# Performance work log

Hardware: AMD Instinct MI355X
Metric: run time of the kernel (lower is better)

## Reference

```python
import jax, jax.numpy as jnp
import numpy as np

K_CLASSES = 5   # num support classes (5-way)
N_SHOT = 5      # supports per class


def setup_inputs() -> dict:
    key = jax.random.key(0)
    k0, k1, k2, k3 = jax.random.split(key, 4)
    b, bs, c, h, w = 32, K_CLASSES * N_SHOT, 512, 14, 14
    dk, dv = 128, 128
    return {
        "support_features": jax.random.normal(k0, (bs, c, h, w), jnp.float32),
        "query_features": jax.random.normal(k1, (b, c, h, w), jnp.float32),
        "support_labels": jnp.repeat(jnp.arange(K_CLASSES), N_SHOT).astype(jnp.int32),
        "W_qk": jax.random.normal(k2, (dk, c), jnp.float32) * 0.02,  # 1x1 conv weight
        "W_v": jax.random.normal(k3, (dv, c), jnp.float32) * 0.02,   # 1x1 conv weight
    }


def reference(support_features, query_features, support_labels, W_qk, W_v):
    scale = 1.0  # 1/temperature, temperature=1.0
    # 1x1 convs == channel-mixing einsums
    query_q = jnp.einsum('bchw,dc->bdhw', query_features, W_qk)
    query_v = jnp.einsum('bchw,dc->bdhw', query_features, W_v)
    supp_k = jnp.einsum('nchw,dc->ndhw', support_features, W_qk)
    supp_v = jnpveinsum = jnp.einsum('nchw,dc->ndhw', support_features, W_v)
    supp_v = jnpveinsum
    b, cv, h, w = query_v.shape

    # similarity over all supports: [b,h,w,n,i,j] (contracts dim_key)
    sim = jnp.einsum('bchw,ncij->bhwnij', query_q, supp_k) * scale

    # per-class masked softmax over the (n,i,j) axes restricted to that class's
    # supports == index_select + softmax in the original loop (labels balanced).
    cls_mask = support_labels[None, :] == jnp.arange(K_CLASSES)[:, None]  # [K,n]
    neg = jnp.finfo(sim.dtype).min
    sim_k = jnp.where(cls_mask[:, None, None, None, :, None, None], sim[None], neg)  # [K,b,h,w,n,i,j]
    attn = jax.nn.softmax(sim_k.reshape(K_CLASSES, b, h, w, -1), axis=-1)
    attn = attn.reshape(sim_k.shape)  # masked-out entries -> exactly 0

    # weighted sum of support values: [K,b,c,h,w]
    out = jnp.einsum('kbhwnij,ncij->kbchw', attn, supp_v)
    prototypes = jnp.transpose(out, (1, 0, 2, 3, 4)).reshape(b, K_CLASSES, -1)  # b k (c h w)
    query_v_flat = query_v.reshape(b, 1, -1)  # b () (c h w)
    return prototypes, query_v_flat
```

## Files before the change

### kernel.cpp

```cpp
#include <hip/hip_runtime.h>
#include <cstdint>
#include <cstddef>

#define NB   32
#define NSUP 25
#define KCLS 5
#define NC   512
#define ND   128
#define NP   196
#define JS   208
#define SHIFT 8.0f

#define KPITCH 272
#define KTILE  (16 * KPITCH)
#define KBUF   (2 * KTILE)
#define VPITCH 80
#define VBUF   (128 * VPITCH)
#define BUFSZ  (KBUF + VBUF)

typedef __attribute__((ext_vector_type(8))) short short8;
typedef __attribute__((ext_vector_type(4))) float floatx4;

__device__ inline short f2bf(float x) {
  union { float f; uint32_t u; } v; v.f = x;
  uint32_t r = (v.u + 0x7FFFu + ((v.u >> 16) & 1u)) >> 16;
  return (short)(r & 0xFFFFu);
}
__device__ inline uint32_t pk2(float a, float b) {
  return (uint32_t)(uint16_t)f2bf(a) | ((uint32_t)(uint16_t)f2bf(b) << 16);
}

__global__ __launch_bounds__(256) void wconv_kernel(
    const float* __restrict__ Wqk, const float* __restrict__ Wv,
    uint16_t* __restrict__ Whi)
{
  const int f = (blockIdx.x * 256 + (int)threadIdx.x) * 8;
  const float* src = (f < ND * NC) ? (Wqk + f) : (Wv + f - ND * NC);
  short8 hv;
  #pragma unroll
  for (int i = 0; i < 8; ++i) hv[i] = f2bf(src[i]);
  *(short8*)(Whi + f) = hv;
}

__global__ __launch_bounds__(256) void gemm_kernel(
    const float* __restrict__ supp, const float* __restrict__ qry,
    const uint16_t* __restrict__ Whi,
    uint16_t* __restrict__ Qt, uint16_t* __restrict__ Kt,
    uint16_t* __restrict__ Vt, float* __restrict__ outVq)
{
  __shared__ uint16_t xs[16 * 520];
  const int bx = blockIdx.x;
  const int t16 = bx % 13, img = bx / 13;
  const int tid = (int)threadIdx.x;
  const int w = tid >> 6, lane = tid & 63, ln = lane & 15, q = lane >> 4;
  const int d0 = w * 32;
  const int p0 = t16 * 16;

  const float* __restrict__ X = (img < NB)
      ? (qry  + (size_t)img * NC * NP)
      : (supp + (size_t)(img - NB) * NC * NP);

  #pragma unroll
  for (int k = 0; k < 4; ++k) {
    const int id = k * 256 + tid;
    const int cp = id >> 2;
    const int pq = id & 3;
    int pg = p0 + pq * 4; if (pg > NP - 4) pg = NP - 4;
    const floatx4 fa = *(const floatx4*)(X + (2 * cp) * NP + pg);
    const floatx4 fb = *(const floatx4*)(X + (2 * cp + 1) * NP + pg);
    #pragma unroll
    for (int i = 0; i < 4; ++i)
      *((uint32_t*)xs + (pq * 4 + i) * 260 + cp) = pk2(fa[i], fb[i]);
  }
  __syncthreads();

  floatx4 aQ[2], aV[2];
  #pragma unroll
  for (int nt = 0; nt < 2; ++nt) {
    aQ[nt] = (floatx4){0.f, 0.f, 0.f, 0.f};
    aV[nt] = (floatx4){0.f, 0.f, 0.f, 0.f};
  }

  for (int ks = 0; ks < 16; ++ks) {
    const short8 xh = *(const short8*)&xs[ln * 520 + ks * 32 + q * 8];
    #pragma unroll
    for (int nt = 0; nt < 2; ++nt) {
      const size_t wr = (size_t)(d0 + nt * 16 + ln) * NC + ks * 32 + q * 8;
      const short8 wqh = *(const short8*)(Whi + wr);
      aQ[nt] = __builtin_amdgcn_mfma_f32_16x16x32_bf16(xh, wqh, aQ[nt], 0, 0, 0);
      const short8 wvh = *(const short8*)(Whi + (size_t)ND * NC + wr);
      aV[nt] = __builtin_amdgcn_mfma_f32_16x16x32_bf16(wvh, xh, aV[nt], 0, 0, 0);
    }
  }

  if (img < NB) {
    #pragma unroll
    for (int nt = 0; nt < 2; ++nt)
      #pragma unroll
      for (int rr = 0; rr < 4; ++rr) {
        const int p = p0 + q * 4 + rr;
        if (p < NP)
          Qt[((size_t)img * NP + p) * ND + d0 + nt * 16 + ln] = (uint16_t)f2bf(aQ[nt][rr]);
      }
  } else {
    const int n = img - NB;
    #pragma unroll
    for (int nt = 0; nt < 2; ++nt)
      #pragma unroll
      for (int rr = 0; rr < 4; ++rr) {
        const int p = p0 + q * 4 + rr;
        Kt[((size_t)n * JS + p) * ND + d0 + nt * 16 + ln] = (uint16_t)f2bf(aQ[nt][rr]);
      }
  }
  const int p = p0 + ln;
  if (img < NB) {
    if (p < NP) {
      #pragma unroll
      for (int nt = 0; nt < 2; ++nt)
        #pragma unroll
        for (int rr = 0; rr < 4; ++rr)
          outVq[((size_t)img * ND + d0 + nt * 16 + q * 4 + rr) * NP + p] = aV[nt][rr];
    }
  } else {
    const int n = img - NB;
    #pragma unroll
    for (int nt = 0; nt < 2; ++nt)
      #pragma unroll
      for (int rr = 0; rr < 4; ++rr)
        Vt[((size_t)n * ND + d0 + nt * 16 + q * 4 + rr) * JS + p] = (uint16_t)f2bf(aV[nt][rr]);
  }
}

__global__ __launch_bounds__(256, 2) void attn_kernel(
    const uint16_t* __restrict__ Qt, const uint16_t* __restrict__ Kt,
    const uint16_t* __restrict__ Vt, const int* __restrict__ labels,
    float* __restrict__ out)
{
  __shared__ __align__(16) char smem[2 * BUFSZ];

  const int bx = blockIdx.x;
  const int pt = bx % 13;
  const int rem = bx / 13;
  const int kc = rem % KCLS;
  const int b0 = (rem / KCLS) * 4;
  const int p0 = pt * 16;
  const int tid = (int)threadIdx.x;
  const int w = tid >> 6, lane = tid & 63, ln = lane & 15, q = lane >> 4;
  const int b = b0 + w;

  const int myl = (lane < NSUP) ? labels[lane] : -1;
  unsigned long long m = __ballot(myl == kc);
  int clsPack = 0;
  #pragma unroll
  for (int s = 0; s < 5; ++s) {
    const int n = (m != 0ull) ? (int)__builtin_ctzll(m) : 0;
    clsPack |= n << (6 * s);
    m &= (m - 1);
  }

  short8 aq[4];
  {
    int p = p0 + ln; if (p > NP - 1) p = NP - 1;
    const uint16_t* base = Qt + ((size_t)b * NP + p) * ND + q * 8;
    #pragma unroll
    for (int ks = 0; ks < 4; ++ks) aq[ks] = *(const short8*)(base + ks * 32);
  }

  floatx4 acc[8];
  #pragma unroll
  for (int dt = 0; dt < 8; ++dt) acc[dt] = (floatx4){0.f, 0.f, 0.f, 0.f};
  float Ssum = 0.f;

  const int alo = (ln + ((q & 1) << 5)) << 2;
  const bool hiTile = (q >= 2);

  int4 pf[4];
  {
    int nk[2], j0k[2], nv[2], jv[2];
    #pragma unroll
    for (int t = 0; t < 2; ++t) {
      const int tile16 = t;
      int s = tile16 / 13;
      j0k[t] = (tile16 - s * 13) * 16;
      if (s > 4) s = 4;
      nk[t] = (clsPack >> (6 * s)) & 63;
    }
    #pragma unroll
    for (int h = 0; h < 2; ++h) {
      const int ch = h * 16;
      int sv = ch / JS, jvv = ch - sv * JS;
      if (sv > 4) { sv = 4; jvv = 192; }
      nv[h] = (clsPack >> (6 * sv)) & 63;
      jv[h] = jvv;
    }
    #pragma unroll
    for (int pass = 0; pass < 4; ++pass) {
      const int slot = pass * 256 + tid;
      if (pass < 2) {
        const int t = slot >> 8, r = (slot >> 4) & 15, sc = slot & 15;
        pf[pass] = *(const int4*)(Kt + ((size_t)(nk[t] * JS + j0k[t] + r)) * ND + sc * 8);
      } else {
        const int vs = slot - 512;
        const int h = vs >> 8, d = (vs >> 1) & 127, sc2 = vs & 1;
        pf[pass] = *(const int4*)(Vt + ((size_t)(nv[h] * ND + d)) * JS + jv[h] + sc2 * 8);
      }
    }
    char* db = smem;
    #pragma unroll
    for (int pass = 0; pass < 4; ++pass) {
      const int slot = pass * 256 + tid;
      if (pass < 2) {
        const int t = slot >> 8, r = (slot >> 4) & 15, sc = slot & 15;
        *(int4*)(db + t * KTILE + r * KPITCH + sc * 16) = pf[pass];
      } else {
        const int vs = slot - 512;
        const int h = vs >> 8, d = (vs >> 1) & 127, sc2 = vs & 1;
        *(int4*)(db + KBUF + d * VPITCH + (h * 2 + sc2) * 16) = pf[pass];
      }
    }
  }
  __syncthreads();

  for (int it = 0; it < 33; ++it) {
    const int nb = it + 1;
    int nk[2], j0k[2], nv[2], jv[2];
    if (nb < 33) {
      #pragma unroll
      for (int t = 0; t < 2; ++t) {
        const int tile16 = nb * 2 + t;
        int s = tile16 / 13;
        j0k[t] = (tile16 - s * 13) * 16;
        if (s > 4) s = 4;
        nk[t] = (clsPack >> (6 * s)) & 63;
      }
      #pragma unroll
      for (int h = 0; h < 2; ++h) {
        const int ch = nb * 32 + h * 16;
        int sv = ch / JS, jvv = ch - sv * JS;
        if (sv > 4) { sv = 4; jvv = 192; }
        nv[h] = (clsPack >> (6 * sv)) & 63;
        jv[h] = jvv;
      }
      #pragma unroll
      for (int pass = 0; pass < 4; ++pass) {
        const int slot = pass * 256 + tid;
        if (pass < 2) {
          const int t = slot >> 8, r = (slot >> 4) & 15, sc = slot & 15;
          pf[pass] = *(const int4*)(Kt + ((size_t)(nk[t] * JS + j0k[t] + r)) * ND + sc * 8);
        } else {
          const int vs = slot - 512;
          const int h = vs >> 8, d = (vs >> 1) & 127, sc2 = vs & 1;
          pf[pass] = *(const int4*)(Vt + ((size_t)(nv[h] * ND + d)) * JS + jv[h] + sc2 * 8);
        }
      }
    }

    const char* kb = smem + (it & 1) * BUFSZ;
    const char* vb = kb + KBUF;

    short8 av[8];
    #pragma unroll
    for (int dt = 0; dt < 8; ++dt)
      av[dt] = *(const short8*)(vb + (dt * 16 + ln) * VPITCH + q * 16);

    short8 bk[2][4];
    #pragma unroll
    for (int t = 0; t < 2; ++t)
      #pragma unroll
      for (int ks = 0; ks < 4; ++ks)
        bk[t][ks] = *(const short8*)(kb + t * KTILE + ln * KPITCH + ks * 64 + q * 16);

    floatx4 e0, e1;
    #pragma unroll
    for (int t = 0; t < 2; ++t) {
      const int tile16 = it * 2 + t;
      const int s = tile16 / 13;
      const int j0 = (tile16 - s * 13) * 16;
      const bool tval = (s < 5);
      floatx4 d4 = {0.f, 0.f, 0.f, 0.f};
      #pragma unroll
      for (int ks = 0; ks < 4; ++ks)
        d4 = __builtin_amdgcn_mfma_f32_16x16x32_bf16(bk[t][ks], aq[ks], d4, 0, 0, 0);
      floatx4 ev;
      #pragma unroll
      for (int r = 0; r < 4; ++r) {
        const int j = j0 + q * 4 + r;
        const float e = (tval && j < NP) ? __expf(d4[r] - SHIFT) : 0.f;
        ev[r] = e;
        Ssum += e;
      }
      if (t == 0) e0 = ev; else e1 = ev;
    }

    short8 bp;
    #pragma unroll
    for (int r = 0; r < 4; ++r) {
      const uint32_t pe = pk2(e0[r], e1[r]);
      const int lo = __builtin_amdgcn_ds_bpermute(alo, (int)pe);
      const int hi = __builtin_amdgcn_ds_bpermute(alo + 64, (int)pe);
      bp[r]     = (short)(uint16_t)(hiTile ? (lo >> 16) : (lo & 0xFFFF));
      bp[4 + r] = (short)(uint16_t)(hiTile ? (hi >> 16) : (hi & 0xFFFF));
    }

    #pragma unroll
    for (int dt = 0; dt < 8; ++dt)
      acc[dt] = __builtin_amdgcn_mfma_f32_16x16x32_bf16(av[dt], bp, acc[dt], 0, 0, 0);

    if (nb < 33) {
      char* db = smem + (nb & 1) * BUFSZ;
      #pragma unroll
      for (int pass = 0; pass < 4; ++pass) {
        const int slot = pass * 256 + tid;
        if (pass < 2) {
          const int t = slot >> 8, r = (slot >> 4) & 15, sc = slot & 15;
          *(int4*)(db + t * KTILE + r * KPITCH + sc * 16) = pf[pass];
        } else {
          const int vs = slot - 512;
          const int h = vs >> 8, d = (vs >> 1) & 127, sc2 = vs & 1;
          *(int4*)(db + KBUF + d * VPITCH + (h * 2 + sc2) * 16) = pf[pass];
        }
      }
    }
    __syncthreads();
  }

  float sv = Ssum;
  sv += __shfl_xor(sv, 16);
  sv += __shfl_xor(sv, 32);
  const float inv = 1.f / sv;
  const int pp = p0 + ln;
  if (pp < NP) {
    float* ob = out + ((size_t)(b * KCLS + kc) * ND + q * 4) * NP + pp;
    #pragma unroll
    for (int dt = 0; dt < 8; ++dt)
      #pragma unroll
      for (int rr = 0; rr < 4; ++rr)
        ob[(size_t)(dt * 16 + rr) * NP] = acc[dt][rr] * inv;
  }
}

extern "C" void kernel_launch(void* const* d_in, const int* in_sizes, int n_in,
                              void* d_out, int out_size, void* d_ws, size_t ws_size,
                              hipStream_t stream) {
  const float* supp   = (const float*)d_in[0];
  const float* qry    = (const float*)d_in[1];
  const int*   labels = (const int*)d_in[2];
  const float* Wqk    = (const float*)d_in[3];
  const float* Wv     = (const float*)d_in[4];
  float* out = (float*)d_out;

  uint16_t* Whi = (uint16_t*)d_ws;
  uint16_t* Qt  = Whi + (size_t)2 * ND * NC;
  uint16_t* Kt  = Qt  + (size_t)NB * NP * ND;
  uint16_t* Vt  = Kt  + (size_t)NSUP * JS * ND;
  float* outVq = out + (size_t)NB * KCLS * ND * NP;

  wconv_kernel<<<64, 256, 0, stream>>>(Wqk, Wv, Whi);
  gemm_kernel<<<741, 256, 0, stream>>>(supp, qry, Whi, Qt, Kt, Vt, outVq);
  attn_kernel<<<520, 256, 0, stream>>>(Qt, Kt, Vt, labels, out);
}
```

Before: 161.4 us.

## Load K/V MFMA fragments directly from global into registers, dropping LDS staging

Replaces the double-buffered shared-memory staging of K and V tiles with per-wave direct global loads of MFMA fragments into registers. Two register sets are ping-ponged so the next chunk is fetched while the current one is computed. This removes LDS writes/reads and all per-iteration __syncthreads, at the cost of each of the four waves redundantly fetching the same K/V data from global/L2 and of higher register pressure.

```diff
diff --git a/kernel.cpp b/kernel.cpp
--- a/kernel.cpp
+++ b/kernel.cpp
@@ -10,13 +10,6 @@
 #define NP   196
 #define JS   208
 #define SHIFT 8.0f
-
-#define KPITCH 272
-#define KTILE  (16 * KPITCH)
-#define KBUF   (2 * KTILE)
-#define VPITCH 80
-#define VBUF   (128 * VPITCH)
-#define BUFSZ  (KBUF + VBUF)
 
 typedef __attribute__((ext_vector_type(8))) short short8;
 typedef __attribute__((ext_vector_type(4))) float floatx4;
@@ -131,13 +124,74 @@
   }
 }
 
+
+#define LOAD_FRAGS(BK, AV, CH) do {                                            \
+    _Pragma("unroll")                                                          \
+    for (int t_ = 0; t_ < 2; ++t_) {                                           \
+      const int tile16_ = (CH) * 2 + t_;                                       \
+      int s_ = tile16_ / 13;                                                   \
+      const int j0_ = (tile16_ - s_ * 13) * 16;                                \
+      if (s_ > 4) s_ = 4;                                                      \
+      const int n_ = (clsPack >> (6 * s_)) & 63;                               \
+      const uint16_t* kr_ = Kt + ((size_t)(n_ * JS + j0_ + ln)) * ND + q * 8;  \
+      _Pragma("unroll")                                                        \
+      for (int ks_ = 0; ks_ < 4; ++ks_)                                        \
+        BK[t_][ks_] = *(const short8*)(kr_ + ks_ * 32);                        \
+    }                                                                          \
+    {                                                                          \
+      const int h_ = q >> 1;                                                   \
+      const int ch_ = (CH) * 32 + h_ * 16;                                     \
+      int sv_ = ch_ / JS, jv_ = ch_ - sv_ * JS;                                \
+      if (sv_ > 4) { sv_ = 4; jv_ = 192; }                                     \
+      const int n_ = (clsPack >> (6 * sv_)) & 63;                              \
+      const uint16_t* vr_ = Vt + ((size_t)n_ * ND + ln) * JS + jv_ + (q & 1) * 8; \
+      _Pragma("unroll")                                                        \
+      for (int dt_ = 0; dt_ < 8; ++dt_)                                        \
+        AV[dt_] = *(const short8*)(vr_ + (size_t)(dt_ * 16) * JS);             \
+    }                                                                          \
+  } while (0)
+
+#define COMPUTE_CHUNK(BK, AV, CH) do {                                         \
+    floatx4 e0_, e1_;                                                          \
+    _Pragma("unroll")                                                          \
+    for (int t_ = 0; t_ < 2; ++t_) {                                           \
+      const int tile16_ = (CH) * 2 + t_;                                       \
+      const int s_ = tile16_ / 13;                                             \
+      const int j0_ = (tile16_ - s_ * 13) * 16;                                \
+      const bool tval_ = (s_ < 5);                                             \
+      floatx4 d4_ = {0.f, 0.f, 0.f, 0.f};                                      \
+      _Pragma("unroll")                                                        \
+      for (int ks_ = 0; ks_ < 4; ++ks_)                                        \
+        d4_ = __builtin_amdgcn_mfma_f32_16x16x32_bf16(BK[t_][ks_], aq[ks_], d4_, 0, 0, 0); \
+      floatx4 ev_;                                                             \
+      _Pragma("unroll")                                                        \
+      for (int r_ = 0; r_ < 4; ++r_) {                                         \
+        const int j_ = j0_ + q * 4 + r_;                                       \
+        const float e_ = (tval_ && j_ < NP) ? __expf(d4_[r_] - SHIFT) : 0.f;   \
+        ev_[r_] = e_;                                                          \
+        Ssum += e_;                                                            \
+      }                                                                        \
+      if (t_ == 0) e0_ = ev_; else e1_ = ev_;                                  \
+    }                                                                          \
+    short8 bp_;                                                                \
+    _Pragma("unroll")                                                          \
+    for (int r_ = 0; r_ < 4; ++r_) {                                           \
+      const uint32_t pe_ = pk2(e0_[r_], e1_[r_]);                              \
+      const int lo_ = __builtin_amdgcn_ds_bpermute(alo, (int)pe_);             \
+      const int hi_ = __builtin_amdgcn_ds_bpermute(alo + 64, (int)pe_);        \
+      bp_[r_]     = (short)(uint16_t)(hiTile ? (lo_ >> 16) : (lo_ & 0xFFFF));  \
+      bp_[4 + r_] = (short)(uint16_t)(hiTile ? (hi_ >> 16) : (hi_ & 0xFFFF));  \
+    }                                                                          \
+    _Pragma("unroll")                                                          \
+    for (int dt_ = 0; dt_ < 8; ++dt_)                                          \
+      acc[dt_] = __builtin_amdgcn_mfma_f32_16x16x32_bf16(AV[dt_], bp_, acc[dt_], 0, 0, 0); \
+  } while (0)
+
 __global__ __launch_bounds__(256, 2) void attn_kernel(
     const uint16_t* __restrict__ Qt, const uint16_t* __restrict__ Kt,
     const uint16_t* __restrict__ Vt, const int* __restrict__ labels,
     float* __restrict__ out)
 {
-  __shared__ __align__(16) char smem[2 * BUFSZ];
-
   const int bx = blockIdx.x;
   const int pt = bx % 13;
   const int rem = bx / 13;
@@ -174,155 +228,15 @@
   const int alo = (ln + ((q & 1) << 5)) << 2;
   const bool hiTile = (q >= 2);
 
-  int4 pf[4];
-  {
-    int nk[2], j0k[2], nv[2], jv[2];
-    #pragma unroll
-    for (int t = 0; t < 2; ++t) {
-      const int tile16 = t;
-      int s = tile16 / 13;
-      j0k[t] = (tile16 - s * 13) * 16;
-      if (s > 4) s = 4;
-      nk[t] = (clsPack >> (6 * s)) & 63;
-    }
-    #pragma unroll
-    for (int h = 0; h < 2; ++h) {
-      const int ch = h * 16;
-      int sv = ch / JS, jvv = ch - sv * JS;
-      if (sv > 4) { sv = 4; jvv = 192; }
-      nv[h] = (clsPack >> (6 * sv)) & 63;
-      jv[h] = jvv;
-    }
-    #pragma unroll
-    for (int pass = 0; pass < 4; ++pass) {
-      const int slot = pass * 256 + tid;
-      if (pass < 2) {
-        const int t = slot >> 8, r = (slot >> 4) & 15, sc = slot & 15;
-        pf[pass] = *(const int4*)(Kt + ((size_t)(nk[t] * JS + j0k[t] + r)) * ND + sc * 8);
-      } else {
-        const int vs = slot - 512;
-        const int h = vs >> 8, d = (vs >> 1) & 127, sc2 = vs & 1;
-        pf[pass] = *(const int4*)(Vt + ((size_t)(nv[h] * ND + d)) * JS + jv[h] + sc2 * 8);
-      }
-    }
-    char* db = smem;
-    #pragma unroll
-    for (int pass = 0; pass < 4; ++pass) {
-      const int slot = pass * 256 + tid;
-      if (pass < 2) {
-        const int t = slot >> 8, r = (slot >> 4) & 15, sc = slot & 15;
-        *(int4*)(db + t * KTILE + r * KPITCH + sc * 16) = pf[pass];
-      } else {
-        const int vs = slot - 512;
-        const int h = vs >> 8, d = (vs >> 1) & 127, sc2 = vs & 1;
-        *(int4*)(db + KBUF + d * VPITCH + (h * 2 + sc2) * 16) = pf[pass];
-      }
-    }
-  }
-  __syncthreads();
-
-  for (int it = 0; it < 33; ++it) {
-    const int nb = it + 1;
-    int nk[2], j0k[2], nv[2], jv[2];
-    if (nb < 33) {
-      #pragma unroll
-      for (int t = 0; t < 2; ++t) {
-        const int tile16 = nb * 2 + t;
-        int s = tile16 / 13;
-        j0k[t] = (tile16 - s * 13) * 16;
-        if (s > 4) s = 4;
-        nk[t] = (clsPack >> (6 * s)) & 63;
-      }
-      #pragma unroll
-      for (int h = 0; h < 2; ++h) {
-        const int ch = nb * 32 + h * 16;
-        int sv = ch / JS, jvv = ch - sv * JS;
-        if (sv > 4) { sv = 4; jvv = 192; }
-        nv[h] = (clsPack >> (6 * sv)) & 63;
-        jv[h] = jvv;
-      }
-      #pragma unroll
-      for (int pass = 0; pass < 4; ++pass) {
-        const int slot = pass * 256 + tid;
-        if (pass < 2) {
-          const int t = slot >> 8, r = (slot >> 4) & 15, sc = slot & 15;
-          pf[pass] = *(const int4*)(Kt + ((size_t)(nk[t] * JS + j0k[t] + r)) * ND + sc * 8);
-        } else {
-          const int vs = slot - 512;
-          const int h = vs >> 8, d = (vs >> 1) & 127, sc2 = vs & 1;
-          pf[pass] = *(const int4*)(Vt + ((size_t)(nv[h] * ND + d)) * JS + jv[h] + sc2 * 8);
-        }
-      }
-    }
-
-    const char* kb = smem + (it & 1) * BUFSZ;
-    const char* vb = kb + KBUF;
-
-    short8 av[8];
-    #pragma unroll
-    for (int dt = 0; dt < 8; ++dt)
-      av[dt] = *(const short8*)(vb + (dt * 16 + ln) * VPITCH + q * 16);
-
-    short8 bk[2][4];
-    #pragma unroll
-    for (int t = 0; t < 2; ++t)
-      #pragma unroll
-      for (int ks = 0; ks < 4; ++ks)
-        bk[t][ks] = *(const short8*)(kb + t * KTILE + ln * KPITCH + ks * 64 + q * 16);
-
-    floatx4 e0, e1;
-    #pragma unroll
-    for (int t = 0; t < 2; ++t) {
-      const int tile16 = it * 2 + t;
-      const int s = tile16 / 13;
-      const int j0 = (tile16 - s * 13) * 16;
-      const bool tval = (s < 5);
-      floatx4 d4 = {0.f, 0.f, 0.f, 0.f};
-      #pragma unroll
-      for (int ks = 0; ks < 4; ++ks)
-        d4 = __builtin_amdgcn_mfma_f32_16x16x32_bf16(bk[t][ks], aq[ks], d4, 0, 0, 0);
-      floatx4 ev;
-      #pragma unroll
-      for (int r = 0; r < 4; ++r) {
-        const int j = j0 + q * 4 + r;
-        const float e = (tval && j < NP) ? __expf(d4[r] - SHIFT) : 0.f;
-        ev[r] = e;
-        Ssum += e;
-      }
-      if (t == 0) e0 = ev; else e1 = ev;
-    }
-
-    short8 bp;
-    #pragma unroll
-    for (int r = 0; r < 4; ++r) {
-      const uint32_t pe = pk2(e0[r], e1[r]);
-      const int lo = __builtin_amdgcn_ds_bpermute(alo, (int)pe);
-      const int hi = __builtin_amdgcn_ds_bpermute(alo + 64, (int)pe);
-      bp[r]     = (short)(uint16_t)(hiTile ? (lo >> 16) : (lo & 0xFFFF));
-      bp[4 + r] = (short)(uint16_t)(hiTile ? (hi >> 16) : (hi & 0xFFFF));
-    }
-
-    #pragma unroll
-    for (int dt = 0; dt < 8; ++dt)
-      acc[dt] = __builtin_amdgcn_mfma_f32_16x16x32_bf16(av[dt], bp, acc[dt], 0, 0, 0);
-
-    if (nb < 33) {
-      char* db = smem + (nb & 1) * BUFSZ;
-      #pragma unroll
-      for (int pass = 0; pass < 4; ++pass) {
-        const int slot = pass * 256 + tid;
-        if (pass < 2) {
-          const int t = slot >> 8, r = (slot >> 4) & 15, sc = slot & 15;
-          *(int4*)(db + t * KTILE + r * KPITCH + sc * 16) = pf[pass];
-        } else {
-          const int vs = slot - 512;
-          const int h = vs >> 8, d = (vs >> 1) & 127, sc2 = vs & 1;
-          *(int4*)(db + KBUF + d * VPITCH + (h * 2 + sc2) * 16) = pf[pass];
-        }
-      }
-    }
-    __syncthreads();
-  }
+  short8 bkA[2][4], avA[8], bkB[2][4], avB[8];
+  LOAD_FRAGS(bkA, avA, 0);
+  for (int it = 0; it < 32; it += 2) {
+    LOAD_FRAGS(bkB, avB, it + 1);
+    COMPUTE_CHUNK(bkA, avA, it);
+    LOAD_FRAGS(bkA, avA, it + 2);
+    COMPUTE_CHUNK(bkB, avB, it + 1);
+  }
+  COMPUTE_CHUNK(bkA, avA, 32);
 
   float sv = Ssum;
   sv += __shfl_xor(sv, 16);
```

Result: slower. 226.9 us (+40.6%).

## Double tile depth per stage and switch LDS to XOR-swizzled layout

Applied to the files above, without the earlier changes.

The attention kernel now stages 64 support positions per pipeline step instead of 32, halving the number of barrier-separated iterations (17 instead of 33). Padded-pitch LDS layouts are replaced with XOR-swizzled layouts and precomputed fragment offsets, and the class pack is made wave-uniform. Tile indices are decoded incrementally with counters instead of divisions. The larger buffers raise LDS use per block to 64KB and increase prefetch registers, which may limit occupancy at two blocks per CU.

```diff
diff --git a/kernel.cpp b/kernel.cpp
--- a/kernel.cpp
+++ b/kernel.cpp
@@ -11,12 +11,9 @@
 #define JS   208
 #define SHIFT 8.0f
 
-#define KPITCH 272
-#define KTILE  (16 * KPITCH)
-#define KBUF   (2 * KTILE)
-#define VPITCH 80
-#define VBUF   (128 * VPITCH)
-#define BUFSZ  (KBUF + VBUF)
+#define KTILE  4096
+#define VBASE  16384
+#define BUFSZ  32768
 
 typedef __attribute__((ext_vector_type(8))) short short8;
 typedef __attribute__((ext_vector_type(4))) float floatx4;
@@ -131,6 +128,35 @@
   }
 }
 
+
+#define DECODE() do {                                                          \
+    _Pragma("unroll")                                                          \
+    for (int t_ = 0; t_ < 4; ++t_) {                                           \
+      dS[t_] = s_ctr; dJ[t_] = j_ctr;                                          \
+      const int sc_ = s_ctr > 4 ? 4 : s_ctr;                                   \
+      dN[t_] = (clsPack >> (6 * sc_)) & 63;                                    \
+      j_ctr += 16; if (j_ctr >= JS) { j_ctr -= JS; s_ctr += 1; }               \
+    }                                                                          \
+  } while (0)
+
+#define ISSUE() do {                                                           \
+    _Pragma("unroll")                                                          \
+    for (int p_ = 0; p_ < 4; ++p_)                                             \
+      pf[p_] = *(const int4*)(Kt + (size_t)(dN[p_] * JS + dJ[p_]) * ND + kinv);\
+    _Pragma("unroll")                                                          \
+    for (int p_ = 0; p_ < 4; ++p_)                                             \
+      pf[4 + p_] = *(const int4*)(Vt + (size_t)dN[p_] * (ND * JS) + dJ[p_] + vinv); \
+  } while (0)
+
+#define STORE() do {                                                           \
+    _Pragma("unroll")                                                          \
+    for (int p_ = 0; p_ < 4; ++p_)                                             \
+      *(int4*)(smem + kstA + p_ * KTILE) = pf[p_];                             \
+    _Pragma("unroll")                                                          \
+    for (int p_ = 0; p_ < 4; ++p_)                                             \
+      *(int4*)(smem + vstA[p_]) = pf[4 + p_];                                  \
+  } while (0)
+
 __global__ __launch_bounds__(256, 2) void attn_kernel(
     const uint16_t* __restrict__ Qt, const uint16_t* __restrict__ Kt,
     const uint16_t* __restrict__ Vt, const int* __restrict__ labels,
@@ -157,6 +183,7 @@
     clsPack |= n << (6 * s);
     m &= (m - 1);
   }
+  clsPack = __builtin_amdgcn_readfirstlane(clsPack);
 
   short8 aq[4];
   {
@@ -174,154 +201,102 @@
   const int alo = (ln + ((q & 1) << 5)) << 2;
   const bool hiTile = (q >= 2);
 
-  int4 pf[4];
-  {
-    int nk[2], j0k[2], nv[2], jv[2];
-    #pragma unroll
-    for (int t = 0; t < 2; ++t) {
-      const int tile16 = t;
-      int s = tile16 / 13;
-      j0k[t] = (tile16 - s * 13) * 16;
-      if (s > 4) s = 4;
-      nk[t] = (clsPack >> (6 * s)) & 63;
+  const int rK = tid >> 4, scK = tid & 15;
+  const int kinv = rK * ND + scK * 8;
+  int kstA = rK * 256 + ((scK * 16) ^ ((rK & 7) << 4));
+  const int dV = tid >> 1, s2V = tid & 1;
+  const int vinv = dV * JS + s2V * 8;
+  int vstA[4];
+  #pragma unroll
+  for (int sub = 0; sub < 4; ++sub)
+    vstA[sub] = VBASE + dV * 128 + ((((sub << 1) + s2V) ^ (dV & 7)) << 4);
+
+  int kfrx[4], vfrx[2];
+  #pragma unroll
+  for (int ks = 0; ks < 4; ++ks)
+    kfrx[ks] = ln * 256 + (((ks << 6) | (q << 4)) ^ ((ln & 7) << 4));
+  #pragma unroll
+  for (int c = 0; c < 2; ++c)
+    vfrx[c] = VBASE + ln * 128 + ((((c << 2) | q) << 4) ^ ((ln & 7) << 4));
+
+  int s_ctr = 0, j_ctr = 0;
+  int dS[4], dJ[4], dN[4], cS[4], cJ[4];
+  int4 pf[8];
+
+  DECODE();
+  ISSUE();
+  STORE();
+  kstA ^= BUFSZ;
+  #pragma unroll
+  for (int i = 0; i < 4; ++i) vstA[i] ^= BUFSZ;
+  #pragma unroll
+  for (int i = 0; i < 4; ++i) { cS[i] = dS[i]; cJ[i] = dJ[i]; }
+  __syncthreads();
+
+  for (int it = 0; it < 17; ++it) {
+    if (it < 16) { DECODE(); ISSUE(); }
+
+    #pragma unroll
+    for (int c = 0; c < 2; ++c) {
+      short8 bk[2][4];
+      #pragma unroll
+      for (int t = 0; t < 2; ++t)
+        #pragma unroll
+        for (int ks = 0; ks < 4; ++ks)
+          bk[t][ks] = *(const short8*)(smem + kfrx[ks] + (c * 2 + t) * KTILE);
+
+      floatx4 e0, e1;
+      #pragma unroll
+      for (int t = 0; t < 2; ++t) {
+        const int tt = c * 2 + t;
+        floatx4 d4 = {0.f, 0.f, 0.f, 0.f};
+        #pragma unroll
+        for (int ks = 0; ks < 4; ++ks)
+          d4 = __builtin_amdgcn_mfma_f32_16x16x32_bf16(bk[t][ks], aq[ks], d4, 0, 0, 0);
+        floatx4 ev;
+        #pragma unroll
+        for (int r = 0; r < 4; ++r) {
+          const int j = cJ[tt] + q * 4 + r;
+          const float e = (cS[tt] < 5 && j < NP) ? __expf(d4[r] - SHIFT) : 0.f;
+          ev[r] = e;
+          Ssum += e;
+        }
+        if (t == 0) e0 = ev; else e1 = ev;
+      }
+
+      short8 bp;
+      #pragma unroll
+      for (int r = 0; r < 4; ++r) {
+        const uint32_t pe = pk2(e0[r], e1[r]);
+        const int lo = __builtin_amdgcn_ds_bpermute(alo, (int)pe);
+        const int hi = __builtin_amdgcn_ds_bpermute(alo + 64, (int)pe);
+        bp[r]     = (short)(uint16_t)(hiTile ? (lo >> 16) : (lo & 0xFFFF));
+        bp[4 + r] = (short)(uint16_t)(hiTile ? (hi >> 16) : (hi & 0xFFFF));
+      }
+
+      short8 av[8];
+      #pragma unroll
+      for (int dt = 0; dt < 8; ++dt)
+        av[dt] = *(const short8*)(smem + vfrx[c] + dt * 2048);
+      #pragma unroll
+      for (int dt = 0; dt < 8; ++dt)
+        acc[dt] = __builtin_amdgcn_mfma_f32_16x16x32_bf16(av[dt], bp, acc[dt], 0, 0, 0);
     }
-    #pragma unroll
-    for (int h = 0; h < 2; ++h) {
-      const int ch = h * 16;
-      int sv = ch / JS, jvv = ch - sv * JS;
-      if (sv > 4) { sv = 4; jvv = 192; }
-      nv[h] = (clsPack >> (6 * sv)) & 63;
-      jv[h] = jvv;
-    }
-    #pragma unroll
-    for (int pass = 0; pass < 4; ++pass) {
-      const int slot = pass * 256 + tid;
-      if (pass < 2) {
-        const int t = slot >> 8, r = (slot >> 4) & 15, sc = slot & 15;
-        pf[pass] = *(const int4*)(Kt + ((size_t)(nk[t] * JS + j0k[t] + r)) * ND + sc * 8);
-      } else {
-        const int vs = slot - 512;
-        const int h = vs >> 8, d = (vs >> 1) & 127, sc2 = vs & 1;
-        pf[pass] = *(const int4*)(Vt + ((size_t)(nv[h] * ND + d)) * JS + jv[h] + sc2 * 8);
-      }
-    }
-    char* db = smem;
-    #pragma unroll
-    for (int pass = 0; pass < 4; ++pass) {
-      const int slot = pass * 256 + tid;
-      if (pass < 2) {
-        const int t = slot >> 8, r = (slot >> 4) & 15, sc = slot & 15;
-        *(int4*)(db + t * KTILE + r * KPITCH + sc * 16) = pf[pass];
-      } else {
-        const int vs = slot - 512;
-        const int h = vs >> 8, d = (vs >> 1) & 127, sc2 = vs & 1;
-        *(int4*)(db + KBUF + d * VPITCH + (h * 2 + sc2) * 16) = pf[pass];
-      }
-    }
-  }
-  __syncthreads();
-
-  for (int it = 0; it < 33; ++it) {
-    const int nb = it + 1;
-    int nk[2], j0k[2], nv[2], jv[2];
-    if (nb < 33) {
-      #pragma unroll
-      for (int t = 0; t < 2; ++t) {
-        const int tile16 = nb * 2 + t;
-        int s = tile16 / 13;
-        j0k[t] = (tile16 - s * 13) * 16;
-        if (s > 4) s = 4;
-        nk[t] = (clsPack >> (6 * s)) & 63;
-      }
-      #pragma unroll
-      for (int h = 0; h < 2; ++h) {
-        const int ch = nb * 32 + h * 16;
-        int sv = ch / JS, jvv = ch - sv * JS;
-        if (sv > 4) { sv = 4; jvv = 192; }
-        nv[h] = (clsPack >> (6 * sv)) & 63;
-        jv[h] = jvv;
-      }
-      #pragma unroll
-      for (int pass = 0; pass < 4; ++pass) {
-        const int slot = pass * 256 + tid;
-        if (pass < 2) {
-          const int t = slot >> 8, r = (slot >> 4) & 15, sc = slot & 15;
-          pf[pass] = *(const int4*)(Kt + ((size_t)(nk[t] * JS + j0k[t] + r)) * ND + sc * 8);
-        } else {
-          const int vs = slot - 512;
-          const int h = vs >> 8, d = (vs >> 1) & 127, sc2 = vs & 1;
-          pf[pass] = *(const int4*)(Vt + ((size_t)(nv[h] * ND + d)) * JS + jv[h] + sc2 * 8);
-        }
-      }
-    }
-
-    const char* kb = smem + (it & 1) * BUFSZ;
-    const char* vb = kb + KBUF;
-
-    short8 av[8];
-    #pragma unroll
-    for (int dt = 0; dt < 8; ++dt)
-      av[dt] = *(const short8*)(vb + (dt * 16 + ln) * VPITCH + q * 16);
-
-    short8 bk[2][4];
-    #pragma unroll
-    for (int t = 0; t < 2; ++t)
-      #pragma unroll
-      for (int ks = 0; ks < 4; ++ks)
-        bk[t][ks] = *(const short8*)(kb + t * KTILE + ln * KPITCH + ks * 64 + q * 16);
-
-    floatx4 e0, e1;
-    #pragma unroll
-    for (int t = 0; t < 2; ++t) {
-      const int tile16 = it * 2 + t;
-      const int s = tile16 / 13;
-      const int j0 = (tile16 - s * 13) * 16;
-      const bool tval = (s < 5);
-      floatx4 d4 = {0.f, 0.f, 0.f, 0.f};
-      #pragma unroll
-      for (int ks = 0; ks < 4; ++ks)
-        d4 = __builtin_amdgcn_mfma_f32_16x16x32_bf16(bk[t][ks], aq[ks], d4, 0, 0, 0);
-      floatx4 ev;
-      #pragma unroll
-      for (int r = 0; r < 4; ++r) {
-        const int j = j0 + q * 4 + r;
-        const float e = (tval && j < NP) ? __expf(d4[r] - SHIFT) : 0.f;
-        ev[r] = e;
-        Ssum += e;
-      }
-      if (t == 0) e0 = ev; else e1 = ev;
-    }
-
-    short8 bp;
-    #pragma unroll
-    for (int r = 0; r < 4; ++r) {
-      const uint32_t pe = pk2(e0[r], e1[r]);
-      const int lo = __builtin_amdgcn_ds_bpermute(alo, (int)pe);
-      const int hi = __builtin_amdgcn_ds_bpermute(alo + 64, (int)pe);
-      bp[r]     = (short)(uint16_t)(hiTile ? (lo >> 16) : (lo & 0xFFFF));
-      bp[4 + r] = (short)(uint16_t)(hiTile ? (hi >> 16) : (hi & 0xFFFF));
-    }
-
-    #pragma unroll
-    for (int dt = 0; dt < 8; ++dt)
-      acc[dt] = __builtin_amdgcn_mfma_f32_16x16x32_bf16(av[dt], bp, acc[dt], 0, 0, 0);
-
-    if (nb < 33) {
-      char* db = smem + (nb & 1) * BUFSZ;
-      #pragma unroll
-      for (int pass = 0; pass < 4; ++pass) {
-        const int slot = pass * 256 + tid;
-        if (pass < 2) {
-          const int t = slot >> 8, r = (slot >> 4) & 15, sc = slot & 15;
-          *(int4*)(db + t * KTILE + r * KPITCH + sc * 16) = pf[pass];
-        } else {
-          const int vs = slot - 512;
-          const int h = vs >> 8, d = (vs >> 1) & 127, sc2 = vs & 1;
-          *(int4*)(db + KBUF + d * VPITCH + (h * 2 + sc2) * 16) = pf[pass];
-        }
-      }
+
+    if (it < 16) {
+      STORE();
+      #pragma unroll
+      for (int i = 0; i < 4; ++i) { cS[i] = dS[i]; cJ[i] = dJ[i]; }
     }
     __syncthreads();
+
+    kstA ^= BUFSZ;
+    #pragma unroll
+    for (int i = 0; i < 4; ++i) vstA[i] ^= BUFSZ;
+    #pragma unroll
+    for (int i = 0; i < 4; ++i) kfrx[i] ^= BUFSZ;
+    #pragma unroll
+    for (int i = 0; i < 2; ++i) vfrx[i] ^= BUFSZ;
   }
 
   float sv = Ssum;
```

After: 169.4 us. +4.9%, slower.

## Split attention reduction over support chunks into two partial blocks plus merge kernel

Applied to the files above, without the earlier changes.

The attention kernel now splits the 33 support chunks of each (batch, class, position-tile) group into two halves of 17. It launches twice as many blocks, and each block writes unnormalized partial accumulators and softmax sums to workspace. A new merge kernel adds the two partials and normalizes into the output. This targets poor wave quantization and long per-block serial loops, since 520 blocks barely exceed one full wave of resident blocks. The price is extra global traffic for the partials and an additional kernel launch. The old single-pass path is kept as a fallback when the workspace is too small.

```diff
diff --git a/kernel.cpp b/kernel.cpp
--- a/kernel.cpp
+++ b/kernel.cpp
@@ -17,6 +17,10 @@
 #define VPITCH 80
 #define VBUF   (128 * VPITCH)
 #define BUFSZ  (KBUF + VBUF)
+
+#define NGRP   (NB * KCLS * 13)
+#define PACC_F ((size_t)NGRP * 2 * 2048)
+#define PSUM_F ((size_t)NGRP * 2 * 16)
 
 typedef __attribute__((ext_vector_type(8))) short short8;
 typedef __attribute__((ext_vector_type(4))) float floatx4;
@@ -131,10 +135,11 @@
   }
 }
 
+template <int NCHUNK, bool PART>
 __global__ __launch_bounds__(256, 2) void attn_kernel(
     const uint16_t* __restrict__ Qt, const uint16_t* __restrict__ Kt,
     const uint16_t* __restrict__ Vt, const int* __restrict__ labels,
-    float* __restrict__ out)
+    float* __restrict__ out, float* __restrict__ pacc, float* __restrict__ psum)
 {
   __shared__ __align__(16) char smem[2 * BUFSZ];
 
@@ -142,7 +147,11 @@
   const int pt = bx % 13;
   const int rem = bx / 13;
   const int kc = rem % KCLS;
-  const int b0 = (rem / KCLS) * 4;
+  const int rest = rem / KCLS;
+  const int bq = PART ? (rest & 7) : rest;
+  const int half = PART ? (rest >> 3) : 0;
+  const int c0 = half * NCHUNK;
+  const int b0 = bq * 4;
   const int p0 = pt * 16;
   const int tid = (int)threadIdx.x;
   const int w = tid >> 6, lane = tid & 63, ln = lane & 15, q = lane >> 4;
@@ -179,7 +188,7 @@
     int nk[2], j0k[2], nv[2], jv[2];
     #pragma unroll
     for (int t = 0; t < 2; ++t) {
-      const int tile16 = t;
+      const int tile16 = c0 * 2 + t;
       int s = tile16 / 13;
       j0k[t] = (tile16 - s * 13) * 16;
       if (s > 4) s = 4;
@@ -187,7 +196,7 @@
     }
     #pragma unroll
     for (int h = 0; h < 2; ++h) {
-      const int ch = h * 16;
+      const int ch = c0 * 32 + h * 16;
       int sv = ch / JS, jvv = ch - sv * JS;
       if (sv > 4) { sv = 4; jvv = 192; }
       nv[h] = (clsPack >> (6 * sv)) & 63;
@@ -221,13 +230,14 @@
   }
   __syncthreads();
 
-  for (int it = 0; it < 33; ++it) {
-    const int nb = it + 1;
+  for (int li = 0; li < NCHUNK; ++li) {
+    const int cc = c0 + li;
+    const int nc = cc + 1;
     int nk[2], j0k[2], nv[2], jv[2];
-    if (nb < 33) {
+    if (li < NCHUNK - 1) {
       #pragma unroll
       for (int t = 0; t < 2; ++t) {
-        const int tile16 = nb * 2 + t;
+        const int tile16 = nc * 2 + t;
         int s = tile16 / 13;
         j0k[t] = (tile16 - s * 13) * 16;
         if (s > 4) s = 4;
@@ -235,7 +245,7 @@
       }
       #pragma unroll
       for (int h = 0; h < 2; ++h) {
-        const int ch = nb * 32 + h * 16;
+        const int ch = nc * 32 + h * 16;
         int sv = ch / JS, jvv = ch - sv * JS;
         if (sv > 4) { sv = 4; jvv = 192; }
         nv[h] = (clsPack >> (6 * sv)) & 63;
@@ -255,7 +265,7 @@
       }
     }
 
-    const char* kb = smem + (it & 1) * BUFSZ;
+    const char* kb = smem + (li & 1) * BUFSZ;
     const char* vb = kb + KBUF;
 
     short8 av[8];
@@ -273,7 +283,7 @@
     floatx4 e0, e1;
     #pragma unroll
     for (int t = 0; t < 2; ++t) {
-      const int tile16 = it * 2 + t;
+      const int tile16 = cc * 2 + t;
       const int s = tile16 / 13;
       const int j0 = (tile16 - s * 13) * 16;
       const bool tval = (s < 5);
@@ -306,8 +316,8 @@
     for (int dt = 0; dt < 8; ++dt)
       acc[dt] = __builtin_amdgcn_mfma_f32_16x16x32_bf16(av[dt], bp, acc[dt], 0, 0, 0);
 
-    if (nb < 33) {
-      char* db = smem + (nb & 1) * BUFSZ;
+    if (li < NCHUNK - 1) {
+      char* db = smem + ((li + 1) & 1) * BUFSZ;
       #pragma unroll
       for (int pass = 0; pass < 4; ++pass) {
         const int slot = pass * 256 + tid;
@@ -327,15 +337,53 @@
   float sv = Ssum;
   sv += __shfl_xor(sv, 16);
   sv += __shfl_xor(sv, 32);
-  const float inv = 1.f / sv;
-  const int pp = p0 + ln;
-  if (pp < NP) {
-    float* ob = out + ((size_t)(b * KCLS + kc) * ND + q * 4) * NP + pp;
+
+  if (PART) {
+    const size_t grp = (((size_t)(b * KCLS + kc)) * 13 + pt) * 2 + half;
+    float* pa = pacc + grp * 2048;
     #pragma unroll
     for (int dt = 0; dt < 8; ++dt)
       #pragma unroll
       for (int rr = 0; rr < 4; ++rr)
-        ob[(size_t)(dt * 16 + rr) * NP] = acc[dt][rr] * inv;
+        pa[(dt * 16 + q * 4 + rr) * 16 + ln] = acc[dt][rr];
+    if (q == 0) psum[grp * 16 + ln] = sv;
+  } else {
+    const float inv = 1.f / sv;
+    const int pp = p0 + ln;
+    if (pp < NP) {
+      float* ob = out + ((size_t)(b * KCLS + kc) * ND + q * 4) * NP + pp;
+      #pragma unroll
+      for (int dt = 0; dt < 8; ++dt)
+        #pragma unroll
+        for (int rr = 0; rr < 4; ++rr)
+          ob[(size_t)(dt * 16 + rr) * NP] = acc[dt][rr] * inv;
+    }
+  }
+}
+
+__global__ __launch_bounds__(256) void merge_kernel(
+    const float* __restrict__ pacc, const float* __restrict__ psum,
+    float* __restrict__ out)
+{
+  const int bx = blockIdx.x;
+  const int pt = bx % 13;
+  const int rem = bx / 13;
+  const int tid = (int)threadIdx.x;
+  const int ln = tid & 15, dr = tid >> 4;
+  const size_t g0 = (((size_t)rem) * 13 + pt) * 2;
+
+  const float s = psum[g0 * 16 + ln] + psum[(g0 + 1) * 16 + ln];
+  const int pp = pt * 16 + ln;
+  if (pp >= NP) return;
+  const float inv = 1.f / s;
+
+  const float* pa0 = pacc + g0 * 2048;
+  const float* pa1 = pacc + (g0 + 1) * 2048;
+  float* ob = out + (size_t)rem * ND * NP + pp;
+  #pragma unroll
+  for (int i = 0; i < 8; ++i) {
+    const int d = dr * 8 + i;
+    ob[(size_t)d * NP] = (pa0[d * 16 + ln] + pa1[d * 16 + ln]) * inv;
   }
 }
 
@@ -353,9 +401,17 @@
   uint16_t* Qt  = Whi + (size_t)2 * ND * NC;
   uint16_t* Kt  = Qt  + (size_t)NB * NP * ND;
   uint16_t* Vt  = Kt  + (size_t)NSUP * JS * ND;
+  float* pacc   = (float*)(Vt + (size_t)NSUP * ND * JS);
+  float* psum   = pacc + PACC_F;
+  const size_t need = (size_t)((char*)(psum + PSUM_F) - (char*)d_ws);
   float* outVq = out + (size_t)NB * KCLS * ND * NP;
 
   wconv_kernel<<<64, 256, 0, stream>>>(Wqk, Wv, Whi);
   gemm_kernel<<<741, 256, 0, stream>>>(supp, qry, Whi, Qt, Kt, Vt, outVq);
-  attn_kernel<<<520, 256, 0, stream>>>(Qt, Kt, Vt, labels, out);
-}
+  if (ws_size >= need) {
+    attn_kernel<17, true><<<1040, 256, 0, stream>>>(Qt, Kt, Vt, labels, out, pacc, psum);
+    merge_kernel<<<2080, 256, 0, stream>>>(pacc, psum, out);
+  } else {
+    attn_kernel<33, false><<<520, 256, 0, stream>>>(Qt, Kt, Vt, labels, out, nullptr, nullptr);
+  }
+}
```

Result: slower. 165.9 us (+2.7%).
